# Performance work log

Hardware: AMD Instinct MI355X
Metric: run time of the kernel (lower is better)

The kernel has to match this reference:

```python
import jax, jax.numpy as jnp
import numpy as np

EPS = 1e-5
GROUPS = 32


def _group_norm(x, w, b):
    # x: [B, C, H, W]
    B, C, H, W = x.shape
    xg = x.reshape(B, GROUPS, (C // GROUPS) * H * W)
    mean = xg.mean(axis=-1, keepdims=True)
    var = xg.var(axis=-1, keepdims=True)
    xn = ((xg - mean) * jax.lax.rsqrt(var + EPS)).reshape(B, C, H, W)
    return xn * w[None, :, None, None] + b[None, :, None, None]


def setup_inputs() -> dict:
    key = jax.random.key(0)
    ks = jax.random.split(key, 8)
    B, C, H, W = 2, 512, 64, 64
    s = 1.0 / np.sqrt(C)
    return {
        "hidden_states": jax.random.normal(ks[0], (B, C, H, W), jnp.float32),
        "gn_weight": jnp.ones((C,), jnp.float32),
        "gn_bias": jnp.zeros((C,), jnp.float32),
        "wq": jax.random.normal(ks[1], (C, C), jnp.float32) * s,
        "bq": jnp.zeros((C,), jnp.float32),
        "wk": jax.random.normal(ks[2], (C, C), jnp.float32) * s,
        "bk": jnp.zeros((C,), jnp.float32),
        "wv": jax.random.normal(ks[3], (C, C), jnp.float32) * s,
        "bv": jnp.zeros((C,), jnp.float32),
        "wo": jax.random.normal(ks[4], (C, C), jnp.float32) * s,
        "bo": jnp.zeros((C,), jnp.float32),
    }


def reference(hidden_states, gn_weight, gn_bias, wq, bq, wk, bk, wv, bv, wo, bo):
    x = hidden_states
    B, C, H, W = x.shape
    residual = x
    h = _group_norm(x, gn_weight, gn_bias)
    # [B, S, C] with S = H*W
    h = h.reshape(B, C, H * W).transpose(0, 2, 1)
    scale = jnp.asarray(C, h.dtype) ** -0.5
    q = (h @ wq.T + bq) * scale          # [B, S, C]
    k = h @ wk.T + bk                    # [B, S, C]
    v = h @ wv.T + bv                    # [B, S, C]
    attn = jax.nn.softmax(jnp.einsum("bsc,btc->bst", q, k), axis=-1)
    o = jnp.einsum("bst,btc->bsc", attn, v)
    o = o @ wo.T + bo
    o = o.transpose(0, 2, 1).reshape(B, C, H, W)
    return o + residual
```

## Files before the change

### kernel.cpp

```cpp
#include <hip/hip_runtime.h>
#include <hip/hip_bf16.h>
#include <stdint.h>

#define S_LEN 4096
#define C_DIM 512
#define NGROUPS 32
#define EPS_GN 1e-5f
#define QSCALE 0.044194173824159216f

typedef float f32x4 __attribute__((ext_vector_type(4)));
typedef float f32x16 __attribute__((ext_vector_type(16)));
typedef __bf16 bf16x8 __attribute__((ext_vector_type(8)));
typedef unsigned short u16;
typedef unsigned int u32;

__device__ __forceinline__ u16 f2bf(float f) {
    union { float f; u32 u; } v; v.f = f;
    u32 r = v.u + 0x7FFFu + ((v.u >> 16) & 1u);
    return (u16)(r >> 16);
}
__device__ __forceinline__ u32 pack2(float a, float b) {
    return (u32)f2bf(a) | ((u32)f2bf(b) << 16);
}

__device__ __forceinline__ void async16(const void* g, void* l) {
    __builtin_amdgcn_global_load_lds((const __attribute__((address_space(1))) u32*)g,
                                     (__attribute__((address_space(3))) u32*)l, 16, 0, 0);
}

#define BARRIER() do { asm volatile("" ::: "memory"); __builtin_amdgcn_s_barrier(); asm volatile("" ::: "memory"); } while (0)
#define WAIT_LGKM0() asm volatile("s_waitcnt lgkmcnt(0)" ::: "memory")
#define WAIT_VM0()   asm volatile("s_waitcnt vmcnt(0)" ::: "memory")

__global__ __launch_bounds__(256) void gn_wconv_kernel(const float* __restrict__ x,
                                                       const float* __restrict__ wq,
                                                       const float* __restrict__ wk,
                                                       const float* __restrict__ wv,
                                                       const float* __restrict__ wo,
                                                       float* __restrict__ stats,
                                                       u16* __restrict__ wb) {
    const int tid = threadIdx.x;
    if (blockIdx.x >= 64) {
        const int i = (blockIdx.x - 64) * 256 + tid;
        const int m = i >> 16;
        const int j = i & 65535;
        const float* src = (m == 0) ? wq : (m == 1) ? wk : (m == 2) ? wv : wo;
        const float4 v = ((const float4*)src)[j];
        ushort4 o;
        o.x = f2bf(v.x); o.y = f2bf(v.y); o.z = f2bf(v.z); o.w = f2bf(v.w);
        ((ushort4*)wb)[i] = o;
        return;
    }
    const int bg = blockIdx.x;
    const float* p = x + (size_t)bg * (16 * S_LEN);
    float s = 0.f, ss = 0.f;
    for (int i = tid; i < (16 * S_LEN) / 4; i += 256) {
        const float4 v = ((const float4*)p)[i];
        s += v.x + v.y + v.z + v.w;
        ss += v.x * v.x + v.y * v.y + v.z * v.z + v.w * v.w;
    }
#pragma unroll
    for (int off = 32; off > 0; off >>= 1) {
        s += __shfl_down(s, off);
        ss += __shfl_down(ss, off);
    }
    __shared__ float rs_[4], rss_[4];
    if ((tid & 63) == 0) { rs_[tid >> 6] = s; rss_[tid >> 6] = ss; }
    __syncthreads();
    if (tid == 0) {
        const float S = rs_[0] + rs_[1] + rs_[2] + rs_[3];
        const float SS = rss_[0] + rss_[1] + rss_[2] + rss_[3];
        const float mean = S * (1.f / 65536.f);
        const float var = SS * (1.f / 65536.f) - mean * mean;
        stats[bg * 2] = mean;
        stats[bg * 2 + 1] = rsqrtf(var + EPS_GN);
    }
}

__global__ __launch_bounds__(256) void hnorm_kernel(const float* __restrict__ x,
                                                    const float* __restrict__ stats,
                                                    const float* __restrict__ gw,
                                                    const float* __restrict__ gb,
                                                    u16* __restrict__ h) {
    __shared__ float tile[32][65];
    const int b = blockIdx.z, c0 = blockIdx.y * 32, s0 = blockIdx.x * 64;
    const int tid = threadIdx.x;
#pragma unroll
    for (int kq = 0; kq < 2; ++kq) {
        const int f = tid + kq * 256;
        const int c = f >> 4, cs = f & 15;
        const float4 v = *(const float4*)(x + ((size_t)(b * C_DIM + c0 + c) * S_LEN + s0 + cs * 4));
        const int g = (c0 + c) >> 4;
        const float mean = stats[(b * NGROUPS + g) * 2];
        const float rstd = stats[(b * NGROUPS + g) * 2 + 1];
        const float a = rstd * gw[c0 + c];
        const float be = gb[c0 + c] - mean * a;
        tile[c][cs * 4 + 0] = v.x * a + be;
        tile[c][cs * 4 + 1] = v.y * a + be;
        tile[c][cs * 4 + 2] = v.z * a + be;
        tile[c][cs * 4 + 3] = v.w * a + be;
    }
    __syncthreads();
#pragma unroll
    for (int kq = 0; kq < 2; ++kq) {
        const int f = tid + kq * 256;
        const int s = f >> 3, c4 = f & 7;
        ushort4 o;
        o.x = f2bf(tile[c4 * 4 + 0][s]);
        o.y = f2bf(tile[c4 * 4 + 1][s]);
        o.z = f2bf(tile[c4 * 4 + 2][s]);
        o.w = f2bf(tile[c4 * 4 + 3][s]);
        *(ushort4*)(h + ((size_t)(b * S_LEN + s0 + s) * C_DIM + c0 + c4 * 4)) = o;
    }
}

template <int MODE>
__global__ __launch_bounds__(256) void proj_kernel(
    const u16* __restrict__ A, const u16* __restrict__ W,
    const float* __restrict__ bias0, const float* __restrict__ bias1,
    const float* __restrict__ bias2,
    u16* __restrict__ oq, u16* __restrict__ ok_, u16* __restrict__ ovT,
    const float* __restrict__ xres, float* __restrict__ out) {
    __shared__ u16 SMEM[128 * 64 * 2];
    u16* const As = SMEM;
    u16* const Bs = SMEM + 8192;

    const int mt = blockIdx.x;
    const int nt = blockIdx.y;
    const int m0 = mt * 128;
    const int which = (MODE == 0) ? (nt >> 2) : 0;
    const int n0 = (MODE == 0) ? ((nt & 3) * 128) : (nt * 128);

    const u16* Ab = A + (size_t)m0 * C_DIM;
    const u16* Bb = W + (size_t)which * (C_DIM * C_DIM) + (size_t)n0 * C_DIM;

    const int tid = threadIdx.x;
    const int w = tid >> 6, l = tid & 63, lr = l & 15, lg = l >> 4;
    const int wr = (w >> 1) * 64, wc = (w & 1) * 64;

    f32x4 acc[4][4];
#pragma unroll
    for (int i = 0; i < 4; ++i)
#pragma unroll
        for (int j = 0; j < 4; ++j) acc[i][j] = (f32x4){0.f, 0.f, 0.f, 0.f};

    for (int ks = 0; ks < 8; ++ks) {
        const int k0 = ks * 64;
#pragma unroll
        for (int i = 0; i < 4; ++i) {
            const int ch = w * 4 + i;
            const int row = ch * 8 + (l >> 3);
            const int sp = (l & 7) ^ (row & 7);
            async16(Ab + (size_t)row * C_DIM + k0 + sp * 8, (void*)(As + ch * 512));
            async16(Bb + (size_t)row * C_DIM + k0 + sp * 8, (void*)(Bs + ch * 512));
        }
        asm volatile("s_waitcnt vmcnt(0)" ::: "memory");
        __syncthreads();
#pragma unroll
        for (int kk = 0; kk < 2; ++kk) {
            bf16x8 af[4], bfr[4];
#pragma unroll
            for (int i = 0; i < 4; ++i) {
                const int row = wr + i * 16 + lr;
                const int p = (kk * 4 + lg) ^ (row & 7);
                af[i] = *(const bf16x8*)(As + row * 64 + p * 8);
            }
#pragma unroll
            for (int j = 0; j < 4; ++j) {
                const int row = wc + j * 16 + lr;
                const int p = (kk * 4 + lg) ^ (row & 7);
                bfr[j] = *(const bf16x8*)(Bs + row * 64 + p * 8);
            }
#pragma unroll
            for (int i = 0; i < 4; ++i)
#pragma unroll
                for (int j = 0; j < 4; ++j)
                    acc[i][j] = __builtin_amdgcn_mfma_f32_16x16x32_bf16(af[i], bfr[j], acc[i][j], 0, 0, 0);
        }
        __syncthreads();
    }

    if (MODE == 0) {
        const float* bias = (which == 0) ? bias0 : (which == 1 ? bias1 : bias2);
        u16* const Ct = SMEM;
#pragma unroll
        for (int j = 0; j < 4; ++j) {
            const int gcl = wc + j * 16 + lr;
            const float bv = bias[n0 + gcl];
#pragma unroll
            for (int i = 0; i < 4; ++i) {
#pragma unroll
                for (int r = 0; r < 4; ++r) {
                    const int grl = wr + i * 16 + lg * 4 + r;
                    float v = acc[i][j][r] + bv;
                    if (which == 0) v *= QSCALE;
                    const u16 hv = f2bf(v);
                    if (which < 2)
                        Ct[grl * 128 + gcl] = hv;
                    else
                        *(u16*)((char*)Ct + gcl * 256 + ((grl * 2) ^ ((gcl & 7) << 4))) = hv;
                }
            }
        }
        __syncthreads();
        if (which < 2) {
            u16* const dst = (which == 0) ? oq : ok_;
#pragma unroll
            for (int it = 0; it < 8; ++it) {
                const int e = it * 256 + tid;
                const int row = e >> 4, c8 = e & 15;
                const uint4 val = *(const uint4*)(Ct + row * 128 + c8 * 8);
                *(uint4*)(dst + (size_t)(m0 + row) * C_DIM + n0 + c8 * 8) = val;
            }
        } else {
            const int b0 = m0 >> 12, s0 = m0 & (S_LEN - 1);
#pragma unroll
            for (int it = 0; it < 8; ++it) {
                const int e = it * 256 + tid;
                const int crow = e >> 4, c8 = e & 15;
                const uint4 val = *(const uint4*)((char*)Ct + crow * 256 + ((c8 * 16) ^ ((crow & 7) << 4)));
                *(uint4*)(ovT + ((size_t)(b0 * C_DIM + n0 + crow)) * S_LEN + s0 + c8 * 8) = val;
            }
        }
    } else {
        float* const Ctf = (float*)SMEM;
        const int b0 = m0 >> 12, s0 = m0 & (S_LEN - 1);
#pragma unroll
        for (int pass = 0; pass < 2; ++pass) {
            if ((w & 1) == pass) {
#pragma unroll
                for (int j = 0; j < 4; ++j) {
                    const int gcl = j * 16 + lr;
                    const float bv = bias0[n0 + pass * 64 + gcl];
#pragma unroll
                    for (int i = 0; i < 4; ++i) {
#pragma unroll
                        for (int r = 0; r < 4; ++r) {
                            const int grl = wr + i * 16 + lg * 4 + r;
                            const float v = acc[i][j][r] + bv;
                            *(float*)((char*)Ctf + gcl * 512 + ((grl * 4) ^ ((gcl & 7) << 4))) = v;
                        }
                    }
                }
            }
            __syncthreads();
#pragma unroll
            for (int it = 0; it < 8; ++it) {
                const int e = it * 256 + tid;
                const int crow = e >> 5, sg = e & 31;
                const f32x4 cv = *(const f32x4*)((char*)Ctf + crow * 512 + ((sg * 16) ^ ((crow & 7) << 4)));
                const size_t gidx = ((size_t)(b0 * C_DIM + n0 + pass * 64 + crow)) * S_LEN + s0 + sg * 4;
                const f32x4 xr = *(const f32x4*)(xres + gidx);
                *(f32x4*)(out + gidx) = cv + xr;
            }
            __syncthreads();
        }
    }
}

__global__ __launch_bounds__(512, 2) void flash_kernel(
    const u16* __restrict__ q, const u16* __restrict__ k, const u16* __restrict__ vT,
    u16* __restrict__ opart, float* __restrict__ ml) {
    __shared__ u16 LDSU[81920];
    float* const Sx = (float*)(LDSU + 65536);

    const int bid = blockIdx.x;
    const int wgid = (bid & 7) * 32 + (bid >> 3);
    const int qt = wgid & 31;
    const int sp = (wgid >> 5) & 3;
    const int b = wgid >> 7;
    const int m0 = qt * 128;
    const int tbeg = sp * 1024;

    const int tid = threadIdx.x;
    const int w = tid >> 6;
    const int l = tid & 63;
    const int rg = w >> 1;
    const int h = w & 1;
    const int ln = l & 31;
    const int hi = l >> 5;

    bf16x8 qf[16];
    {
        const u16* qrow = q + ((size_t)(b * S_LEN) + m0 + rg * 32 + ln) * C_DIM + h * 256 + hi * 8;
#pragma unroll
        for (int cc = 0; cc < 16; ++cc)
            qf[cc] = *(const bf16x8*)(qrow + cc * 16);
    }

    f32x16 oacc[8];
#pragma unroll
    for (int dt = 0; dt < 8; ++dt)
#pragma unroll
        for (int r = 0; r < 16; ++r) oacc[dt][r] = 0.f;
    float rm = -3.0e38f, rl = 0.f;

    const u16* kbase = k + (size_t)b * S_LEN * C_DIM;
    const u16* vbase = vT + (size_t)b * C_DIM * S_LEN;

#pragma unroll
    for (int i = 0; i < 4; ++i) {
        const int row = w * 4 + i;
        async16(kbase + (size_t)(tbeg + row) * C_DIM + ((l ^ (row & 7)) * 8),
                (void*)(LDSU + row * 512));
    }
#pragma unroll
    for (int i = 0; i < 4; ++i) {
        const int ch = w * 4 + i;
        const int d0 = ch * 16;
        const int d = d0 + (l >> 2);
        const int g = (l & 3) ^ ((d >> 1) & 3);
        async16(vbase + (size_t)d * S_LEN + tbeg + g * 8, (void*)(LDSU + 32768 + d0 * 32));
    }
    WAIT_VM0();
    BARRIER();

    for (int step = 0; step < 32; ++step) {
        const int t0 = tbeg + step * 32;
        const u16* kcur = LDSU + (step & 1) * 16384;
        const u16* vcur = LDSU + 32768 + (step & 1) * 16384;

        if (step < 31) {
            u16* knxt = LDSU + ((step + 1) & 1) * 16384;
#pragma unroll
            for (int i = 0; i < 4; ++i) {
                const int row = w * 4 + i;
                async16(kbase + (size_t)(t0 + 32 + row) * C_DIM + ((l ^ (row & 7)) * 8),
                        (void*)(knxt + row * 512));
            }
        }

        f32x16 sa;
#pragma unroll
        for (int r = 0; r < 16; ++r) sa[r] = 0.f;
        __builtin_amdgcn_s_setprio(1);
#pragma unroll
        for (int cc = 0; cc < 16; ++cc) {
            const int g = h * 32 + cc * 2 + hi;
            const bf16x8 af = *(const bf16x8*)(kcur + ln * 512 + ((g ^ (ln & 7)) * 8));
            sa = __builtin_amdgcn_mfma_f32_32x32x16_bf16(af, qf[cc], sa, 0, 0, 0);
        }
        __builtin_amdgcn_s_setprio(0);

        {
            float* swb = Sx + w * 1024 + l * 4;
#pragma unroll
            for (int c = 0; c < 4; ++c)
                *(f32x4*)(swb + c * 256) = (f32x4){sa[c * 4 + 0], sa[c * 4 + 1], sa[c * 4 + 2], sa[c * 4 + 3]};
            if (step < 31) { asm volatile("s_waitcnt vmcnt(4) lgkmcnt(0)" ::: "memory"); }
            else           { asm volatile("s_waitcnt vmcnt(0) lgkmcnt(0)" ::: "memory"); }
            BARRIER();
            const float* prb = Sx + (w ^ 1) * 1024 + l * 4;
#pragma unroll
            for (int c = 0; c < 4; ++c) {
                const f32x4 pv = *(const f32x4*)(prb + c * 256);
                sa[c * 4 + 0] += pv[0];
                sa[c * 4 + 1] += pv[1];
                sa[c * 4 + 2] += pv[2];
                sa[c * 4 + 3] += pv[3];
            }
        }

        if (step < 31) {
            u16* vnxt = LDSU + 32768 + ((step + 1) & 1) * 16384;
#pragma unroll
            for (int i = 0; i < 4; ++i) {
                const int ch = w * 4 + i;
                const int d0 = ch * 16;
                const int d = d0 + (l >> 2);
                const int g = (l & 3) ^ ((d >> 1) & 3);
                async16(vbase + (size_t)d * S_LEN + t0 + 32 + g * 8, (void*)(vnxt + d0 * 32));
            }
        }

        float t8[8];
#pragma unroll
        for (int r = 0; r < 8; ++r) t8[r] = fmaxf(sa[r], sa[r + 8]);
#pragma unroll
        for (int r = 0; r < 4; ++r) t8[r] = fmaxf(t8[r], t8[r + 4]);
        float pm = fmaxf(fmaxf(t8[0], t8[1]), fmaxf(t8[2], t8[3]));
        pm = fmaxf(pm, __shfl_xor(pm, 32));
        if (!__all(pm <= rm + 8.f)) {
            const float mn = fmaxf(rm, pm);
            const float al = __expf(rm - mn);
            rl *= al;
#pragma unroll
            for (int dt = 0; dt < 8; ++dt)
#pragma unroll
                for (int r = 0; r < 16; ++r) oacc[dt][r] *= al;
            rm = mn;
        }
#pragma unroll
        for (int r = 0; r < 16; ++r) sa[r] = __expf(sa[r] - rm);
        {
            float s8[8];
#pragma unroll
            for (int r = 0; r < 8; ++r) s8[r] = sa[r] + sa[r + 8];
#pragma unroll
            for (int r = 0; r < 4; ++r) s8[r] += s8[r + 4];
            float rs = (s8[0] + s8[1]) + (s8[2] + s8[3]);
            rs += __shfl_xor(rs, 32);
            rl += rs;
        }

        u32 wv[8], pw[8];
#pragma unroll
        for (int s4 = 0; s4 < 4; ++s4) {
            asm("v_cvt_pk_bf16_f32 %0, %1, %2" : "=v"(wv[s4 * 2 + 0]) : "v"(sa[s4 * 4 + 0]), "v"(sa[s4 * 4 + 1]));
            asm("v_cvt_pk_bf16_f32 %0, %1, %2" : "=v"(wv[s4 * 2 + 1]) : "v"(sa[s4 * 4 + 2]), "v"(sa[s4 * 4 + 3]));
        }
#pragma unroll
        for (int j = 0; j < 8; ++j) pw[j] = __shfl_xor((int)wv[j], 32);
        union { u32 u[4]; bf16x8 v; } pb0, pb1;
        pb0.u[0] = hi ? pw[2] : wv[0];
        pb0.u[1] = hi ? pw[3] : wv[1];
        pb0.u[2] = hi ? wv[2] : pw[0];
        pb0.u[3] = hi ? wv[3] : pw[1];
        pb1.u[0] = hi ? pw[6] : wv[4];
        pb1.u[1] = hi ? pw[7] : wv[5];
        pb1.u[2] = hi ? wv[6] : pw[4];
        pb1.u[3] = hi ? wv[7] : pw[5];

        __builtin_amdgcn_s_setprio(1);
#pragma unroll
        for (int dt = 0; dt < 8; ++dt) {
            const int d = h * 256 + dt * 32 + ln;
#pragma unroll
            for (int kk = 0; kk < 2; ++kk) {
                const int slot = (kk * 2 + hi) ^ ((d >> 1) & 3);
                const bf16x8 vf = *(const bf16x8*)(vcur + d * 32 + slot * 8);
                oacc[dt] = __builtin_amdgcn_mfma_f32_32x32x16_bf16(vf, kk ? pb1.v : pb0.v, oacc[dt], 0, 0, 0);
            }
        }
        __builtin_amdgcn_s_setprio(0);

        asm volatile("s_waitcnt vmcnt(4) lgkmcnt(0)" ::: "memory");
        BARRIER();
    }

    const float inv = 1.f / rl;
    u16* const Ot = LDSU;
    {
        const int qq = rg * 32 + ln;
#pragma unroll
        for (int dt = 0; dt < 8; ++dt) {
#pragma unroll
            for (int u = 0; u < 8; ++u) {
                const int d = h * 256 + dt * 32 + (((2 * u) & 3) + 8 * (u >> 1) + 4 * hi);
                const u32 word = pack2(oacc[dt][2 * u] * inv, oacc[dt][2 * u + 1] * inv);
                const int byte = qq * 1024 + ((d * 2) ^ ((qq & 7) << 4));
                *(u32*)((char*)Ot + byte) = word;
            }
        }
    }
    if (h == 0 && hi == 0) {
        float* mlp = ml + (size_t)((b * 4 + sp) * 2) * S_LEN;
        mlp[m0 + rg * 32 + ln] = rm;
        mlp[S_LEN + m0 + rg * 32 + ln] = rl;
    }
    WAIT_LGKM0();
    BARRIER();
    {
        u16* od = opart + ((size_t)((b * 4 + sp) * S_LEN) + m0) * C_DIM;
#pragma unroll
        for (int i = 0; i < 16; ++i) {
            const int qq = w * 16 + i;
            const int byte = qq * 1024 + ((l * 16) ^ ((qq & 7) << 4));
            const uint4 tv = *(const uint4*)((char*)Ot + byte);
            *(uint4*)(od + (size_t)qq * C_DIM + l * 8) = tv;
        }
    }
}

__global__ __launch_bounds__(256) void merge_kernel(const u16* __restrict__ opart,
                                                    const float* __restrict__ ml,
                                                    u16* __restrict__ o) {
    const int row = blockIdx.x;
    const int b = row >> 12, s = row & 4095;
    float mi[4], li[4];
#pragma unroll
    for (int i = 0; i < 4; ++i) {
        const float* mlp = ml + (size_t)((b * 4 + i) * 2) * S_LEN;
        mi[i] = mlp[s];
        li[i] = mlp[S_LEN + s];
    }
    float mm = fmaxf(fmaxf(mi[0], mi[1]), fmaxf(mi[2], mi[3]));
    float wsum = 0.f, wi[4];
#pragma unroll
    for (int i = 0; i < 4; ++i) { wi[i] = __expf(mi[i] - mm) * li[i]; wsum += wi[i]; }
    const float invw = 1.f / wsum;
#pragma unroll
    for (int i = 0; i < 4; ++i) wi[i] *= invw;

    const int c = threadIdx.x * 2;
    float a0 = 0.f, a1 = 0.f;
#pragma unroll
    for (int i = 0; i < 4; ++i) {
        const u16* p = opart + ((size_t)((b * 4 + i) * S_LEN) + s) * C_DIM + c;
        const ushort2 uu = *(const ushort2*)p;
        union { u32 u; float f; } c0, c1;
        c0.u = (u32)uu.x << 16; c1.u = (u32)uu.y << 16;
        a0 += wi[i] * c0.f;
        a1 += wi[i] * c1.f;
    }
    u16* orow = o + (size_t)row * C_DIM;
    ushort2 ov;
    ov.x = f2bf(a0); ov.y = f2bf(a1);
    *(ushort2*)(orow + c) = ov;
}

__global__ void sentinel_kernel(float* out) {
    if (threadIdx.x == 0 && blockIdx.x == 0) out[0] = 12345.0f;
}

extern "C" void kernel_launch(void* const* d_in, const int* in_sizes, int n_in,
                              void* d_out, int out_size, void* d_ws, size_t ws_size,
                              hipStream_t stream) {
    (void)in_sizes; (void)n_in; (void)out_size;
    const float* x  = (const float*)d_in[0];
    const float* gw = (const float*)d_in[1];
    const float* gb = (const float*)d_in[2];
    const float* wq = (const float*)d_in[3];
    const float* bq = (const float*)d_in[4];
    const float* wk = (const float*)d_in[5];
    const float* bk = (const float*)d_in[6];
    const float* wv = (const float*)d_in[7];
    const float* bv = (const float*)d_in[8];
    const float* wo = (const float*)d_in[9];
    const float* bo = (const float*)d_in[10];
    float* out = (float*)d_out;

    const size_t REQ = 69469184;
    if (ws_size < REQ) {
        sentinel_kernel<<<1, 64, 0, stream>>>(out);
        return;
    }
    char* ws = (char*)d_ws;
    float* stats = (float*)ws;
    u16* wb  = (u16*)(ws + 1024);
    u16* h   = (u16*)(ws + 1024 + 2097152);
    u16* qb  = h + (size_t)8192 * 512;
    u16* kb  = qb + (size_t)8192 * 512;
    u16* vTb = kb + (size_t)8192 * 512;
    u16* opart = vTb + (size_t)8192 * 512;
    float* ml = (float*)((char*)opart + (size_t)33554432);
    u16* ob = h;

    gn_wconv_kernel<<<1088, 256, 0, stream>>>(x, wq, wk, wv, wo, stats, wb);
    hnorm_kernel<<<dim3(64, 16, 2), 256, 0, stream>>>(x, stats, gw, gb, h);
    proj_kernel<0><<<dim3(64, 12), 256, 0, stream>>>(h, wb, bq, bk, bv, qb, kb, vTb,
                                                     nullptr, nullptr);
    flash_kernel<<<256, 512, 0, stream>>>(qb, kb, vTb, opart, ml);
    merge_kernel<<<8192, 256, 0, stream>>>(opart, ml, ob);
    proj_kernel<1><<<dim3(64, 4), 256, 0, stream>>>(ob, wb + (size_t)3 * 262144, bo, nullptr,
                                                    nullptr, nullptr, nullptr, nullptr, x, out);
}
```

Baseline: 191.4 us.

## Split group-norm stats into partial blocks and double-buffer projection GEMM K-loop

The group-norm statistics pass now uses 256 blocks that each write partial sums, and the normalization kernel combines four partials per group, so the reduction is spread over more of the GPU. The projection GEMM switches from single-buffered 64-wide K stages with two barriers per step to double-buffered 32-wide stages. Each next stage is prefetched asynchronously while MFMAs run on the current one, with one barrier per step. This aims to hide global-load latency, at the cost of more iterations and a new swizzle pattern.

```diff
diff --git a/kernel.cpp b/kernel.cpp
--- a/kernel.cpp
+++ b/kernel.cpp
@@ -37,11 +37,11 @@
                                                        const float* __restrict__ wk,
                                                        const float* __restrict__ wv,
                                                        const float* __restrict__ wo,
-                                                       float* __restrict__ stats,
+                                                       float* __restrict__ pstats,
                                                        u16* __restrict__ wb) {
     const int tid = threadIdx.x;
-    if (blockIdx.x >= 64) {
-        const int i = (blockIdx.x - 64) * 256 + tid;
+    if (blockIdx.x >= 256) {
+        const int i = (blockIdx.x - 256) * 256 + tid;
         const int m = i >> 16;
         const int j = i & 65535;
         const float* src = (m == 0) ? wq : (m == 1) ? wk : (m == 2) ? wv : wo;
@@ -51,11 +51,11 @@
         ((ushort4*)wb)[i] = o;
         return;
     }
-    const int bg = blockIdx.x;
-    const float* p = x + (size_t)bg * (16 * S_LEN);
+    const float* p = x + (size_t)blockIdx.x * 16384;
     float s = 0.f, ss = 0.f;
-    for (int i = tid; i < (16 * S_LEN) / 4; i += 256) {
-        const float4 v = ((const float4*)p)[i];
+#pragma unroll
+    for (int it = 0; it < 16; ++it) {
+        const float4 v = ((const float4*)p)[it * 256 + tid];
         s += v.x + v.y + v.z + v.w;
         ss += v.x * v.x + v.y * v.y + v.z * v.z + v.w * v.w;
     }
@@ -68,17 +68,13 @@
     if ((tid & 63) == 0) { rs_[tid >> 6] = s; rss_[tid >> 6] = ss; }
     __syncthreads();
     if (tid == 0) {
-        const float S = rs_[0] + rs_[1] + rs_[2] + rs_[3];
-        const float SS = rss_[0] + rss_[1] + rss_[2] + rss_[3];
-        const float mean = S * (1.f / 65536.f);
-        const float var = SS * (1.f / 65536.f) - mean * mean;
-        stats[bg * 2] = mean;
-        stats[bg * 2 + 1] = rsqrtf(var + EPS_GN);
+        pstats[blockIdx.x * 2 + 0] = rs_[0] + rs_[1] + rs_[2] + rs_[3];
+        pstats[blockIdx.x * 2 + 1] = rss_[0] + rss_[1] + rss_[2] + rss_[3];
     }
 }
 
 __global__ __launch_bounds__(256) void hnorm_kernel(const float* __restrict__ x,
-                                                    const float* __restrict__ stats,
+                                                    const float* __restrict__ pstats,
                                                     const float* __restrict__ gw,
                                                     const float* __restrict__ gb,
                                                     u16* __restrict__ h) {
@@ -91,8 +87,11 @@
         const int c = f >> 4, cs = f & 15;
         const float4 v = *(const float4*)(x + ((size_t)(b * C_DIM + c0 + c) * S_LEN + s0 + cs * 4));
         const int g = (c0 + c) >> 4;
-        const float mean = stats[(b * NGROUPS + g) * 2];
-        const float rstd = stats[(b * NGROUPS + g) * 2 + 1];
+        const float* pp = pstats + (size_t)(b * NGROUPS + g) * 8;
+        const float S  = (pp[0] + pp[2]) + (pp[4] + pp[6]);
+        const float SS = (pp[1] + pp[3]) + (pp[5] + pp[7]);
+        const float mean = S * (1.f / 65536.f);
+        const float rstd = rsqrtf(SS * (1.f / 65536.f) - mean * mean + EPS_GN);
         const float a = rstd * gw[c0 + c];
         const float be = gb[c0 + c] - mean * a;
         tile[c][cs * 4 + 0] = v.x * a + be;
@@ -121,9 +120,7 @@
     const float* __restrict__ bias2,
     u16* __restrict__ oq, u16* __restrict__ ok_, u16* __restrict__ ovT,
     const float* __restrict__ xres, float* __restrict__ out) {
-    __shared__ u16 SMEM[128 * 64 * 2];
-    u16* const As = SMEM;
-    u16* const Bs = SMEM + 8192;
+    __shared__ u16 SMEM[16384];
 
     const int mt = blockIdx.x;
     const int nt = blockIdx.y;
@@ -144,41 +141,55 @@
 #pragma unroll
         for (int j = 0; j < 4; ++j) acc[i][j] = (f32x4){0.f, 0.f, 0.f, 0.f};
 
-    for (int ks = 0; ks < 8; ++ks) {
-        const int k0 = ks * 64;
+#define STAGE(P, K0)                                                                     \
+    do {                                                                                 \
+        u16* const Asp_ = SMEM + (P) * 8192;                                             \
+        u16* const Bsp_ = Asp_ + 4096;                                                   \
+        _Pragma("unroll") for (int i = 0; i < 2; ++i) {                                  \
+            const int ch = w * 2 + i;                                                    \
+            const int row = ch * 16 + (l >> 2);                                          \
+            const int sg = (l & 3) ^ ((row >> 1) & 3);                                   \
+            async16(Ab + (size_t)row * C_DIM + (K0) + sg * 8, (void*)(Asp_ + ch * 512)); \
+        }                                                                                \
+        _Pragma("unroll") for (int i = 0; i < 2; ++i) {                                  \
+            const int ch = w * 2 + i;                                                    \
+            const int row = ch * 16 + (l >> 2);                                          \
+            const int sg = (l & 3) ^ ((row >> 1) & 3);                                   \
+            async16(Bb + (size_t)row * C_DIM + (K0) + sg * 8, (void*)(Bsp_ + ch * 512)); \
+        }                                                                                \
+    } while (0)
+
+    STAGE(0, 0);
+    WAIT_VM0();
+    BARRIER();
+
+    for (int t = 0; t < 16; ++t) {
+        const int p = t & 1;
+        if (t < 15) STAGE(p ^ 1, (t + 1) * 32);
+        const u16* Asp = SMEM + p * 8192;
+        const u16* Bsp = Asp + 4096;
+        bf16x8 af[4], bfr[4];
 #pragma unroll
         for (int i = 0; i < 4; ++i) {
-            const int ch = w * 4 + i;
-            const int row = ch * 8 + (l >> 3);
-            const int sp = (l & 7) ^ (row & 7);
-            async16(Ab + (size_t)row * C_DIM + k0 + sp * 8, (void*)(As + ch * 512));
-            async16(Bb + (size_t)row * C_DIM + k0 + sp * 8, (void*)(Bs + ch * 512));
-        }
-        asm volatile("s_waitcnt vmcnt(0)" ::: "memory");
-        __syncthreads();
-#pragma unroll
-        for (int kk = 0; kk < 2; ++kk) {
-            bf16x8 af[4], bfr[4];
-#pragma unroll
-            for (int i = 0; i < 4; ++i) {
-                const int row = wr + i * 16 + lr;
-                const int p = (kk * 4 + lg) ^ (row & 7);
-                af[i] = *(const bf16x8*)(As + row * 64 + p * 8);
-            }
-#pragma unroll
-            for (int j = 0; j < 4; ++j) {
-                const int row = wc + j * 16 + lr;
-                const int p = (kk * 4 + lg) ^ (row & 7);
-                bfr[j] = *(const bf16x8*)(Bs + row * 64 + p * 8);
-            }
-#pragma unroll
-            for (int i = 0; i < 4; ++i)
-#pragma unroll
-                for (int j = 0; j < 4; ++j)
-                    acc[i][j] = __builtin_amdgcn_mfma_f32_16x16x32_bf16(af[i], bfr[j], acc[i][j], 0, 0, 0);
-        }
-        __syncthreads();
-    }
+            const int row = wr + i * 16 + lr;
+            const int g = lg ^ ((row >> 1) & 3);
+            af[i] = *(const bf16x8*)(Asp + row * 32 + g * 8);
+        }
+#pragma unroll
+        for (int j = 0; j < 4; ++j) {
+            const int row = wc + j * 16 + lr;
+            const int g = lg ^ ((row >> 1) & 3);
+            bfr[j] = *(const bf16x8*)(Bsp + row * 32 + g * 8);
+        }
+#pragma unroll
+        for (int i = 0; i < 4; ++i)
+#pragma unroll
+            for (int j = 0; j < 4; ++j)
+                acc[i][j] = __builtin_amdgcn_mfma_f32_16x16x32_bf16(af[i], bfr[j], acc[i][j], 0, 0, 0);
+        asm volatile("s_waitcnt vmcnt(0) lgkmcnt(0)" ::: "memory");
+        BARRIER();
+    }
+#undef STAGE
 
     if (MODE == 0) {
         const float* bias = (which == 0) ? bias0 : (which == 1 ? bias1 : bias2);
@@ -536,7 +547,6 @@
         return;
     }
     char* ws = (char*)d_ws;
-    float* stats = (float*)ws;
     u16* wb  = (u16*)(ws + 1024);
     u16* h   = (u16*)(ws + 1024 + 2097152);
     u16* qb  = h + (size_t)8192 * 512;
@@ -544,10 +554,11 @@
     u16* vTb = kb + (size_t)8192 * 512;
     u16* opart = vTb + (size_t)8192 * 512;
     float* ml = (float*)((char*)opart + (size_t)33554432);
+    float* pstats = ml;
     u16* ob = h;
 
-    gn_wconv_kernel<<<1088, 256, 0, stream>>>(x, wq, wk, wv, wo, stats, wb);
-    hnorm_kernel<<<dim3(64, 16, 2), 256, 0, stream>>>(x, stats, gw, gb, h);
+    gn_wconv_kernel<<<1280, 256, 0, stream>>>(x, wq, wk, wv, wo, pstats, wb);
+    hnorm_kernel<<<dim3(64, 16, 2), 256, 0, stream>>>(x, pstats, gw, gb, h);
     proj_kernel<0><<<dim3(64, 12), 256, 0, stream>>>(h, wb, bq, bk, bv, qb, kb, vTb,
                                                      nullptr, nullptr);
     flash_kernel<<<256, 512, 0, stream>>>(qb, kb, vTb, opart, ml);
```

New measurement: 173.2 us. 9.5% less time.
